# Kernel optimization log

Measured on AMD Instinct MI355X. Metric: run time of the kernel, lower is better.

Reference implementation:

```python
import jax, jax.numpy as jnp
import numpy as np

B, N_NODE, E_PER, C, HID, HEADS, IN, NL = 16, 1024, 8192, 16, 128, 4, 32, 2
N = B * N_NODE
NEG_SLOPE = 0.2


def setup_inputs() -> dict:
    key = jax.random.key(0)
    ks = jax.random.split(key, 16)
    obs = jax.random.normal(ks[0], (N, IN), jnp.float32)
    # per-graph random edges, guaranteed no self-loops (GATv2Conv re-adds them once)
    src_l = jax.random.randint(ks[1], (B, E_PER), 0, N_NODE)
    off = jax.random.randint(ks[2], (B, E_PER), 1, N_NODE)
    dst_l = (src_l + off) % N_NODE
    base = (jnp.arange(B) * N_NODE)[:, None]
    edge_index = jnp.stack([(src_l + base).reshape(-1), (dst_l + base).reshape(-1)]).astype(jnp.int32)

    def lin(k, fi, fo):
        return (jax.random.normal(k, (fi, fo), jnp.float32) / np.sqrt(fi)).astype(jnp.float32)

    def gat(k):
        sk = jax.random.split(k, 3)
        return {
            'Wl': (jax.random.normal(sk[0], (NL, HID, HEADS * HID), jnp.float32) / np.sqrt(HID)),
            'bl': jnp.zeros((NL, HEADS * HID), jnp.float32),
            'Wr': (jax.random.normal(sk[1], (NL, HID, HEADS * HID), jnp.float32) / np.sqrt(HID)),
            'br': jnp.zeros((NL, HEADS * HID), jnp.float32),
            'att': (jax.random.normal(sk[2], (NL, HEADS, HID), jnp.float32) / np.sqrt(HID)),
            'bias': jnp.zeros((NL, HID), jnp.float32),
            'g': jnp.ones((NL, HID), jnp.float32),
            'beta': jnp.zeros((NL, HID), jnp.float32),
        }

    inp = {'obs': obs, 'edge_index': edge_index, 'n_node': N_NODE,
           'emb_W': lin(ks[3], IN, HID), 'emb_b': jnp.zeros((HID,), jnp.float32),
           'pool_W': lin(ks[4], HID, C), 'pool_b': jnp.zeros((C,), jnp.float32),
           'mlp_W1': lin(ks[5], HID, 4 * HID), 'mlp_b1': jnp.zeros((4 * HID,), jnp.float32),
           'mlp_W2': lin(ks[6], 4 * HID, HID), 'mlp_b2': jnp.zeros((HID,), jnp.float32)}
    for nm, d in (('low', gat(ks[7])), ('high', gat(ks[8]))):
        for k2, v in d.items():
            inp[nm + '_' + k2] = v
    return inp


def _layer_norm(x, g, b):
    mu = x.mean(-1, keepdims=True)
    v = jnp.mean((x - mu) ** 2, -1, keepdims=True)
    return (x - mu) / jnp.sqrt(v + 1e-5) * g + b


def _gatv2(x, src, dst, Wl, bl, Wr, br, att, bias):
    # GATv2Conv: heads H, concat=False (mean over heads), eval mode (no dropout)
    n = x.shape[0]
    H, D = att.shape
    xl = (x @ Wl + bl).reshape(n, H, D)  # source transform (lin_l)
    xr = (x @ Wr + br).reshape(n, H, D)  # target transform (lin_r)
    e = jax.nn.leaky_relu(xl[src] + xr[dst], NEG_SLOPE)  # [E,H,D]
    logit = jnp.einsum('ehd,hd->eh', e, att)
    m = jax.ops.segment_max(logit, dst, num_segments=n)
    p = jnp.exp(logit - m[dst])
    z = jax.ops.segment_sum(p, dst, num_segments=n)
    alpha = p / z[dst]
    out = jax.ops.segment_sum(alpha[:, :, None] * xl[src], dst, num_segments=n)
    return out.mean(axis=1) + bias


def _gat_stack(h, src, dst, Wl, bl, Wr, br, att, bias, g, beta):
    h_res = h
    nl = Wl.shape[0]
    for j in range(nl):
        h_in = h
        h = _gatv2(h, src, dst, Wl[j], bl[j], Wr[j], br[j], att[j], bias[j])
        h = _layer_norm(h, g[j], beta[j])
        if j != nl - 1:
            h = jax.nn.silu(h)
        h = h + h_in  # use_res=True
    return h + h_res


def _forward(obs, edge_index, n_node, emb_W, emb_b, pool_W, pool_b, mlp_W1, mlp_b1, mlp_W2, mlp_b2,
             low_Wl, low_bl, low_Wr, low_br, low_att, low_bias, low_g, low_beta,
             high_Wl, high_bl, high_Wr, high_br, high_att, high_bias, high_g, high_beta):
    n = obs.shape[0]
    h = obs @ emb_W + emb_b
    hh = h
    # low-level edges + self-loops (GATv2Conv add_self_loops; input has none)
    loops = jnp.arange(n, dtype=edge_index.dtype)
    src = jnp.concatenate([edge_index[0], loops])
    dst = jnp.concatenate([edge_index[1], loops])
    h = _gat_stack(h, src, dst, low_Wl, low_bl, low_Wr, low_br, low_att, low_bias, low_g, low_beta)
    # soft pooling
    pooling = jax.nn.softmax(h @ pool_W + pool_b, axis=-1)  # dim=1 == last dim on 2D
    b = n // n_node
    c = pooling.shape[-1]
    s = pooling.reshape(b, n_node, c)
    count = jnp.maximum(s.sum(axis=1), 1e-5)  # sT @ ones, clamp_min(1e-5)
    Hf = jnp.einsum('bnc,bnd->bcd', s, h.reshape(b, n_node, -1)) / count[:, :, None]
    Hf = Hf.reshape(b * c, -1)
    # high-level: fully connected per-graph cluster edges (self-loops already present once)
    hr = jnp.repeat(jnp.arange(c, dtype=jnp.int32), c)
    hc = jnp.tile(jnp.arange(c, dtype=jnp.int32), c)
    offb = (jnp.arange(b, dtype=jnp.int32) * c)[:, None]
    hsrc = (hr[None, :] + offb).reshape(-1)
    hdst = (hc[None, :] + offb).reshape(-1)
    Hf = _gat_stack(Hf, hsrc, hdst, high_Wl, high_bl, high_Wr, high_br, high_att, high_bias, high_g, high_beta)
    # unpool + residual MLP (BaseMLP flat=True: hidden=4*HID, Tanh, residual)
    l_H = jnp.einsum('bnc,bcd->bnd', s, Hf.reshape(b, c, -1)).reshape(n, -1)
    x = l_H + hh
    return jnp.tanh(x @ mlp_W1 + mlp_b1) @ mlp_W2 + mlp_b2 + x


def reference(obs, edge_index, n_node, emb_W, emb_b, pool_W, pool_b, mlp_W1, mlp_b1, mlp_W2, mlp_b2,
              low_Wl, low_bl, low_Wr, low_br, low_att, low_bias, low_g, low_beta,
              high_Wl, high_bl, high_Wr, high_br, high_att, high_bias, high_g, high_beta):
    return _forward(obs, edge_index, n_node, emb_W, emb_b, pool_W, pool_b, mlp_W1, mlp_b1, mlp_W2, mlp_b2,
                    low_Wl, low_bl, low_Wr, low_br, low_att, low_bias, low_g, low_beta,
                    high_Wl, high_bl, high_Wr, high_br, high_att, high_bias, high_g, high_beta)
```

## Files before the change

kernel.cpp:

```cpp
#include <hip/hip_runtime.h>
#include <math.h>

#define NTOT  16384
#define NNODE 1024

typedef unsigned short u16;
typedef unsigned short u16x8 __attribute__((ext_vector_type(8)));
typedef short s16x8 __attribute__((ext_vector_type(8)));
typedef float f32x4 __attribute__((ext_vector_type(4)));

static __device__ __forceinline__ float b2f(u16 u) {
  return __uint_as_float(((unsigned)u) << 16);
}
static __device__ __forceinline__ u16 f2b(float f) {
  unsigned x = __float_as_uint(f);
  return (u16)((x + 0x7FFFu + ((x >> 16) & 1u)) >> 16);
}

__global__ __launch_bounds__(64) void emb_k(const float* __restrict__ obs,
    const float* __restrict__ W, const float* __restrict__ b,
    float* __restrict__ h, float* __restrict__ hh, u16* __restrict__ h_bf)
{
  int n = blockIdx.x, l = threadIdx.x;
  __shared__ float ob[32];
  if (l < 32) ob[l] = obs[n * 32 + l];
  __syncthreads();
  float a0 = b[l], a1 = b[64 + l];
  #pragma unroll
  for (int k = 0; k < 32; ++k) {
    float o = ob[k];
    a0 = fmaf(o, W[k * 128 + l], a0);
    a1 = fmaf(o, W[k * 128 + 64 + l], a1);
  }
  size_t base = (size_t)n * 128;
  h[base + l] = a0;  h[base + 64 + l] = a1;
  hh[base + l] = a0; hh[base + 64 + l] = a1;
  h_bf[base + l] = f2b(a0); h_bf[base + 64 + l] = f2b(a1);
}

__global__ void hist_k(const int* __restrict__ ei, int E0, int* __restrict__ deg)
{
  int i = blockIdx.x * blockDim.x + threadIdx.x;
  int ET = E0 + NTOT;
  if (i < ET) {
    int d = (i < E0) ? ei[E0 + i] : (i - E0);
    atomicAdd(&deg[d], 1);
  }
}

__global__ __launch_bounds__(256) void scan_k(const int* __restrict__ deg,
    int* __restrict__ off, int* __restrict__ cursor)
{
  __shared__ int part[256];
  int t = threadIdx.x;
  int base = t * 64;
  int sum = 0;
  for (int i = 0; i < 64; ++i) sum += deg[base + i];
  part[t] = sum;
  __syncthreads();
  if (t == 0) {
    int run = 0;
    for (int i = 0; i < 256; ++i) { int v = part[i]; part[i] = run; run += v; }
  }
  __syncthreads();
  int run = part[t];
  for (int i = 0; i < 64; ++i) {
    off[base + i] = run; cursor[base + i] = run;
    run += deg[base + i];
  }
  if (t == 255) off[NTOT] = run;
}

__global__ void scat_k(const int* __restrict__ ei, int E0,
    int* __restrict__ cursor, int* __restrict__ csr_src)
{
  int i = blockIdx.x * blockDim.x + threadIdx.x;
  int ET = E0 + NTOT;
  if (i < ET) {
    int s, d;
    if (i < E0) { s = ei[i]; d = ei[E0 + i]; } else { s = d = i - E0; }
    int pos = atomicAdd(&cursor[d], 1);
    csr_src[pos] = s;
  }
}

__global__ void hi_k(int* __restrict__ hi_off, int* __restrict__ hi_src)
{
  int t = threadIdx.x;
  hi_off[t] = t * 16;
  if (t == 0) hi_off[256] = 4096;
  for (int i = t; i < 4096; i += 256) {
    int u = i >> 4;
    hi_src[i] = (u & ~15) + (i & 15);
  }
}

__global__ void wq_k(const float* __restrict__ W, u16* __restrict__ out,
                     int K, int N, int total)
{
  int idx = blockIdx.x * 256 + threadIdx.x;
  if (idx >= total) return;
  int kn = K * N;
  int m = idx / kn, r = idx - m * kn;
  int n = r / K, k = r - n * K;
  out[idx] = f2b(W[(size_t)m * kn + (size_t)k * N + n]);
}

__global__ void wq2_k(const float* __restrict__ Wl, const float* __restrict__ Wr,
                      u16* __restrict__ out, int total)
{
  int idx = blockIdx.x * 256 + threadIdx.x;
  if (idx >= total) return;
  int m = idx >> 17;
  int r = idx & 131071;
  int n = r >> 7, k = r & 127;
  const float* W = (n < 512) ? Wl : Wr;
  out[idx] = f2b(W[(size_t)m * 65536 + (size_t)k * 512 + (n & 511)]);
}

__global__ __launch_bounds__(256) void gemm_bf16(
    const u16* __restrict__ A, const u16* __restrict__ Bt,
    const float* __restrict__ bias0, const float* __restrict__ bias1,
    float* __restrict__ Cf, u16* __restrict__ Cb0, u16* __restrict__ Cb1,
    const float* __restrict__ res,
    int M, int K, int N, int Nsplit, int act)
{
  __shared__ u16 Al[128][128];
  __shared__ u16 Bl[128][128];
  const int tid = threadIdx.x;
  const int bm = blockIdx.x * 128, bn = blockIdx.y * 128;
  const int w = tid >> 6, l = tid & 63;
  const int fr = l & 15;
  const int kg = l >> 4;
  const int sr = tid >> 1;
  const int sh = (tid & 1) << 3;

  f32x4 acc[2][8];
  #pragma unroll
  for (int a = 0; a < 2; ++a)
    #pragma unroll
    for (int b = 0; b < 8; ++b)
      acc[a][b] = (f32x4){0.f, 0.f, 0.f, 0.f};

  for (int k0 = 0; k0 < K; k0 += 128) {
    __syncthreads();
    const u16* As = A + (size_t)(bm + sr) * K + k0 + (sh << 3);
    const u16* Bs = Bt + (size_t)(bn + sr) * K + k0 + (sh << 3);
    #pragma unroll
    for (int i = 0; i < 8; ++i) {
      int gs = (sh + i) ^ (sr & 7);
      *(uint4*)&Al[sr][gs << 3] = *(const uint4*)(As + (i << 3));
    }
    #pragma unroll
    for (int i = 0; i < 8; ++i) {
      int gs = (sh + i) ^ (sr & 7);
      *(uint4*)&Bl[sr][gs << 3] = *(const uint4*)(Bs + (i << 3));
    }
    __syncthreads();
    #pragma unroll
    for (int ks = 0; ks < 4; ++ks) {
      const int g = (ks << 2) + kg;
      const int ar0 = w * 32 + fr, ar1 = ar0 + 16;
      s16x8 a0 = *(const s16x8*)&Al[ar0][(g ^ (ar0 & 7)) << 3];
      s16x8 a1 = *(const s16x8*)&Al[ar1][(g ^ (ar1 & 7)) << 3];
      #pragma unroll
      for (int nr = 0; nr < 8; ++nr) {
        const int br = nr * 16 + fr;
        s16x8 bb = *(const s16x8*)&Bl[br][(g ^ (br & 7)) << 3];
        acc[0][nr] = __builtin_amdgcn_mfma_f32_16x16x32_bf16(a0, bb, acc[0][nr], 0, 0, 0);
        acc[1][nr] = __builtin_amdgcn_mfma_f32_16x16x32_bf16(a1, bb, acc[1][nr], 0, 0, 0);
      }
    }
  }

  #pragma unroll
  for (int mr = 0; mr < 2; ++mr) {
    const int row0 = bm + w * 32 + mr * 16 + (kg << 2);
    #pragma unroll
    for (int nr = 0; nr < 8; ++nr) {
      const int col = bn + nr * 16 + fr;
      const int half = (col >= Nsplit);
      const int c2 = half ? col - Nsplit : col;
      const int str = half ? (N - Nsplit) : Nsplit;
      const float bb = half ? bias1[c2] : bias0[c2];
      u16* cb = half ? Cb1 : Cb0;
      #pragma unroll
      for (int j = 0; j < 4; ++j) {
        float v = acc[mr][nr][j] + bb;
        if (act) v = tanhf(v);
        size_t o = (size_t)(row0 + j) * str + c2;
        if (res) v += res[o];
        if (Cf) Cf[o] = v;
        if (cb) cb[o] = f2b(v);
      }
    }
  }
}

static __device__ __forceinline__ void edge_step(
    u16x8 vv, bool valid, const float* xrr, const float* attr,
    float& m, float& z, float* acc)
{
  float xv[8];
  #pragma unroll
  for (int i = 0; i < 8; ++i) xv[i] = b2f(vv[i]);
  float part = 0.f;
  #pragma unroll
  for (int i = 0; i < 8; ++i) {
    float v = xv[i] + xrr[i];
    part = fmaf(fmaxf(v, 0.2f * v), attr[i], part);
  }
  part += __shfl_xor(part, 1); part += __shfl_xor(part, 2);
  part += __shfl_xor(part, 4); part += __shfl_xor(part, 8);
  if (!valid) part = -1e30f;
  float mn = fmaxf(m, part);
  float sc = __expf(m - mn);
  float p  = __expf(part - mn);
  z = z * sc + p;
  #pragma unroll
  for (int i = 0; i < 8; ++i) acc[i] = fmaf(acc[i], sc, p * xv[i]);
  m = mn;
}

__global__ __launch_bounds__(64) void gat_agg2(
    const u16* __restrict__ xl, const u16* __restrict__ xr,
    const int* __restrict__ off, const int* __restrict__ srcs,
    const float* __restrict__ att, const float* __restrict__ bias,
    const float* __restrict__ g, const float* __restrict__ beta,
    float* __restrict__ h, u16* __restrict__ h_bf,
    const float* __restrict__ res2, int do_silu, int swz)
{
  int b = blockIdx.x, l = threadIdx.x;
  int dst0;
  if (swz) {
    int xcd = b & 7, i = b >> 3;
    dst0 = (((xcd << 1) + (i >> 9)) << 10) | ((i & 511) << 1);
  } else dst0 = b << 1;
  const int dst1 = dst0 + 1;

  float attr[8];
  {
    const float4 a0 = *(const float4*)(att + l * 8);
    const float4 a1 = *(const float4*)(att + l * 8 + 4);
    attr[0] = a0.x; attr[1] = a0.y; attr[2] = a0.z; attr[3] = a0.w;
    attr[4] = a1.x; attr[5] = a1.y; attr[6] = a1.z; attr[7] = a1.w;
  }
  float xrr0[8], xrr1[8];
  {
    u16x8 v0 = *(const u16x8*)(xr + (size_t)dst0 * 512 + l * 8);
    u16x8 v1 = *(const u16x8*)(xr + (size_t)dst1 * 512 + l * 8);
    #pragma unroll
    for (int i = 0; i < 8; ++i) { xrr0[i] = b2f(v0[i]); xrr1[i] = b2f(v1[i]); }
  }
  const int s0 = off[dst0], n0 = off[dst0 + 1] - s0;
  const int s1 = off[dst1], n1 = off[dst1 + 1] - s1;
  const int nmax = n0 > n1 ? n0 : n1;

  int ni0 = (n0 > 1) ? srcs[s0 + 1] : 0;
  int ni1 = (n1 > 1) ? srcs[s1 + 1] : 0;
  u16x8 v0 = *(const u16x8*)(xl + (size_t)srcs[s0] * 512 + l * 8);
  u16x8 v1 = *(const u16x8*)(xl + (size_t)srcs[s1] * 512 + l * 8);

  float m0 = -1e30f, z0 = 0.f, acc0[8] = {};
  float m1 = -1e30f, z1 = 0.f, acc1[8] = {};

  for (int e = 0; e < nmax; ++e) {
    u16x8 c0 = v0, c1 = v1;
    if (e + 1 < nmax) {
      v0 = *(const u16x8*)(xl + (size_t)ni0 * 512 + l * 8);
      v1 = *(const u16x8*)(xl + (size_t)ni1 * 512 + l * 8);
      if (e + 2 < n0) ni0 = srcs[s0 + e + 2];
      if (e + 2 < n1) ni1 = srcs[s1 + e + 2];
    }
    edge_step(c0, e < n0, xrr0, attr, m0, z0, acc0);
    edge_step(c1, e < n1, xrr1, attr, m1, z1, acc1);
  }

  const int d0 = (l & 15) * 8;
  float o0[8], o1[8];
  const float inv0 = 0.25f / z0, inv1 = 0.25f / z1;
  #pragma unroll
  for (int i = 0; i < 8; ++i) {
    float v = acc0[i] * inv0;
    v += __shfl_xor(v, 16); v += __shfl_xor(v, 32);
    o0[i] = v + bias[d0 + i];
    float w2 = acc1[i] * inv1;
    w2 += __shfl_xor(w2, 16); w2 += __shfl_xor(w2, 32);
    o1[i] = w2 + bias[d0 + i];
  }
  float sa = 0.f, sb = 0.f;
  #pragma unroll
  for (int i = 0; i < 8; ++i) { sa += o0[i]; sb += o1[i]; }
  sa += __shfl_xor(sa, 1); sa += __shfl_xor(sa, 2);
  sa += __shfl_xor(sa, 4); sa += __shfl_xor(sa, 8);
  sb += __shfl_xor(sb, 1); sb += __shfl_xor(sb, 2);
  sb += __shfl_xor(sb, 4); sb += __shfl_xor(sb, 8);
  const float mu0 = sa * (1.f / 128.f), mu1 = sb * (1.f / 128.f);
  float va = 0.f, vb = 0.f;
  #pragma unroll
  for (int i = 0; i < 8; ++i) {
    float d = o0[i] - mu0; va += d * d;
    float e = o1[i] - mu1; vb += e * e;
  }
  va += __shfl_xor(va, 1); va += __shfl_xor(va, 2);
  va += __shfl_xor(va, 4); va += __shfl_xor(va, 8);
  vb += __shfl_xor(vb, 1); vb += __shfl_xor(vb, 2);
  vb += __shfl_xor(vb, 4); vb += __shfl_xor(vb, 8);
  const float rstd0 = rsqrtf(va * (1.f / 128.f) + 1e-5f);
  const float rstd1 = rsqrtf(vb * (1.f / 128.f) + 1e-5f);

  const float* oo = (l < 16) ? o0 : o1;
  const float mu = (l < 16) ? mu0 : mu1;
  const float rstd = (l < 16) ? rstd0 : rstd1;
  const int dd = (l < 16) ? dst0 : dst1;
  if (l < 32) {
    size_t base = (size_t)dd * 128 + d0;
    float4 r0 = *(const float4*)(h + base);
    float4 r1 = *(const float4*)(h + base + 4);
    float rr[8] = {r0.x, r0.y, r0.z, r0.w, r1.x, r1.y, r1.z, r1.w};
    if (res2) {
      float4 q0 = *(const float4*)(res2 + base);
      float4 q1 = *(const float4*)(res2 + base + 4);
      rr[0] += q0.x; rr[1] += q0.y; rr[2] += q0.z; rr[3] += q0.w;
      rr[4] += q1.x; rr[5] += q1.y; rr[6] += q1.z; rr[7] += q1.w;
    }
    float out[8];
    u16x8 hb;
    #pragma unroll
    for (int i = 0; i < 8; ++i) {
      float y = (oo[i] - mu) * rstd * g[d0 + i] + beta[d0 + i];
      if (do_silu) y = y / (1.f + __expf(-y));
      out[i] = y + rr[i];
      hb[i] = f2b(out[i]);
    }
    *(float4*)(h + base) = make_float4(out[0], out[1], out[2], out[3]);
    *(float4*)(h + base + 4) = make_float4(out[4], out[5], out[6], out[7]);
    *(u16x8*)(h_bf + base) = hb;
  }
}

__global__ __launch_bounds__(256) void pool_k(const float* __restrict__ h,
    const float* __restrict__ W, const float* __restrict__ b, float* __restrict__ s)
{
  __shared__ float hs[16 * 130];
  __shared__ float Ws[128 * 16];
  int t = threadIdx.x;
  int n0 = blockIdx.x * 16;
  #pragma unroll
  for (int i = 0; i < 8; ++i) {
    int idx = t + 256 * i;
    hs[(idx >> 7) * 130 + (idx & 127)] = h[(size_t)n0 * 128 + idx];
    Ws[idx] = W[idx];
  }
  __syncthreads();
  int nl = t >> 4, c = t & 15;
  float acc = b[c];
  for (int k = 0; k < 128; ++k) acc = fmaf(hs[nl * 130 + k], Ws[k * 16 + c], acc);
  float mx = acc;
  mx = fmaxf(mx, __shfl_xor(mx, 1)); mx = fmaxf(mx, __shfl_xor(mx, 2));
  mx = fmaxf(mx, __shfl_xor(mx, 4)); mx = fmaxf(mx, __shfl_xor(mx, 8));
  float p = __expf(acc - mx), sum = p;
  sum += __shfl_xor(sum, 1); sum += __shfl_xor(sum, 2);
  sum += __shfl_xor(sum, 4); sum += __shfl_xor(sum, 8);
  s[(size_t)(n0 + nl) * 16 + c] = p / sum;
}

#define HF_CHUNK 32
#define HF_NCH   32
__global__ __launch_bounds__(256) void hfp_k(const float* __restrict__ s,
    const float* __restrict__ h, float* __restrict__ part, float* __restrict__ cpart)
{
  __shared__ float ss[HF_CHUNK][16];
  __shared__ float hs[HF_CHUNK][128];
  int b = blockIdx.x >> 5, chunk = blockIdx.x & 31;
  int n0 = b * NNODE + chunk * HF_CHUNK;
  int t = threadIdx.x;
  if (t < 128) {
    float4 v = *(const float4*)(s + (size_t)(n0 + (t >> 2)) * 16 + (t & 3) * 4);
    *(float4*)&ss[t >> 2][(t & 3) * 4] = v;
  }
  #pragma unroll
  for (int i = 0; i < 4; ++i) {
    int idx = t + 256 * i;
    int row = idx >> 5, c4 = (idx & 31) * 4;
    *(float4*)&hs[row][c4] = *(const float4*)(h + (size_t)(n0 + row) * 128 + c4);
  }
  __syncthreads();
  int d = t & 127, cg = (t >> 7) * 8;
  float acc[8] = {};
  for (int n = 0; n < HF_CHUNK; ++n) {
    float hv = hs[n][d];
    #pragma unroll
    for (int i = 0; i < 8; ++i) acc[i] = fmaf(ss[n][cg + i], hv, acc[i]);
  }
  float* po = part + (size_t)chunk * 32768 + (size_t)(b * 16 + cg) * 128 + d;
  #pragma unroll
  for (int i = 0; i < 8; ++i) po[i * 128] = acc[i];
  if (t < 16) {
    float c = 0.f;
    #pragma unroll
    for (int n = 0; n < HF_CHUNK; ++n) c += ss[n][t];
    cpart[chunk * 256 + b * 16 + t] = c;
  }
}

__global__ __launch_bounds__(256) void hfr_k(const float* __restrict__ part,
    const float* __restrict__ cpart, float* __restrict__ Hf,
    float* __restrict__ HfRes, u16* __restrict__ Hf_bf)
{
  int o = blockIdx.x * 256 + threadIdx.x;
  int bc = o >> 7;
  float a = 0.f, cnt = 0.f;
  #pragma unroll 8
  for (int ch = 0; ch < HF_NCH; ++ch) {
    a += part[(size_t)ch * 32768 + o];
    cnt += cpart[ch * 256 + bc];
  }
  float v = a / fmaxf(cnt, 1e-5f);
  Hf[o] = v; HfRes[o] = v; Hf_bf[o] = f2b(v);
}

__global__ __launch_bounds__(64) void unpool_k(const float* __restrict__ s,
    const float* __restrict__ Hf, const float* __restrict__ hh,
    float* __restrict__ x, u16* __restrict__ x_bf)
{
  int n = blockIdx.x, l = threadIdx.x;
  int b = n >> 10;
  float a0 = 0.f, a1 = 0.f;
  #pragma unroll
  for (int c = 0; c < 16; ++c) {
    float sv = s[(size_t)n * 16 + c];
    const float* hp = Hf + (size_t)((b << 4) + c) * 128;
    a0 = fmaf(sv, hp[l], a0);
    a1 = fmaf(sv, hp[64 + l], a1);
  }
  size_t base = (size_t)n * 128;
  float v0 = a0 + hh[base + l], v1 = a1 + hh[base + 64 + l];
  x[base + l] = v0; x[base + 64 + l] = v1;
  x_bf[base + l] = f2b(v0); x_bf[base + 64 + l] = f2b(v1);
}

extern "C" void kernel_launch(void* const* d_in, const int* in_sizes, int n_in,
                              void* d_out, int out_size, void* d_ws, size_t ws_size,
                              hipStream_t stream) {
  (void)n_in; (void)out_size; (void)ws_size;
  const float* obs    = (const float*)d_in[0];
  const int*   ei     = (const int*)d_in[1];
  const float* emb_W  = (const float*)d_in[3];
  const float* emb_b  = (const float*)d_in[4];
  const float* pool_W = (const float*)d_in[5];
  const float* pool_b = (const float*)d_in[6];
  const float* mlp_W1 = (const float*)d_in[7];
  const float* mlp_b1 = (const float*)d_in[8];
  const float* mlp_W2 = (const float*)d_in[9];
  const float* mlp_b2 = (const float*)d_in[10];
  const float* lWl = (const float*)d_in[11]; const float* lbl = (const float*)d_in[12];
  const float* lWr = (const float*)d_in[13]; const float* lbr = (const float*)d_in[14];
  const float* latt = (const float*)d_in[15]; const float* lbias = (const float*)d_in[16];
  const float* lg = (const float*)d_in[17]; const float* lbeta = (const float*)d_in[18];
  const float* hWl = (const float*)d_in[19]; const float* hbl = (const float*)d_in[20];
  const float* hWr = (const float*)d_in[21]; const float* hbr = (const float*)d_in[22];
  const float* hatt = (const float*)d_in[23]; const float* hbias = (const float*)d_in[24];
  const float* hg = (const float*)d_in[25]; const float* hbeta = (const float*)d_in[26];

  const int E0 = in_sizes[1] / 2;
  const int ET = E0 + NTOT;

  char* p = (char*)d_ws;
  auto alloc = [&](size_t bytes) -> void* {
    void* q = (void*)p;
    p += (bytes + 255) & ~(size_t)255;
    return q;
  };
  float* h      = (float*)alloc((size_t)NTOT * 128 * 4);
  float* hh     = (float*)alloc((size_t)NTOT * 128 * 4);
  u16*   h_bf   = (u16*)alloc((size_t)NTOT * 128 * 2);
  u16*   xl_bf  = (u16*)alloc((size_t)NTOT * 512 * 2);
  u16*   xr_bf  = (u16*)alloc((size_t)NTOT * 512 * 2);
  u16*   x_bf   = (u16*)alloc((size_t)NTOT * 128 * 2);
  float* s      = (float*)alloc((size_t)NTOT * 16 * 4);
  float* Hf     = (float*)alloc(256 * 128 * 4);
  float* HfRes  = (float*)alloc(256 * 128 * 4);
  u16*   Hf_bf  = (u16*)alloc(256 * 128 * 2);
  u16*   hxl    = (u16*)alloc(256 * 512 * 2);
  u16*   hxr    = (u16*)alloc(256 * 512 * 2);
  float* hfPart = (float*)alloc((size_t)HF_NCH * 32768 * 4);
  float* hfCnt  = (float*)alloc((size_t)HF_NCH * 256 * 4);
  u16*   lWT    = (u16*)alloc(2 * 1024 * 128 * 2);
  u16*   hWT    = (u16*)alloc(2 * 1024 * 128 * 2);
  u16*   W1T    = (u16*)alloc(512 * 128 * 2);
  u16*   W2T    = (u16*)alloc(128 * 512 * 2);
  int* deg      = (int*)alloc((size_t)NTOT * 4);
  int* off      = (int*)alloc((size_t)(NTOT + 1) * 4);
  int* cursor   = (int*)alloc((size_t)NTOT * 4);
  int* csr      = (int*)alloc((size_t)ET * 4);
  int* hi_off   = (int*)alloc(257 * 4);
  int* hi_src   = (int*)alloc(4096 * 4);
  u16* t_bf     = xl_bf;

  wq2_k<<<(2 * 131072 + 255) / 256, 256, 0, stream>>>(lWl, lWr, lWT, 2 * 131072);
  wq2_k<<<(2 * 131072 + 255) / 256, 256, 0, stream>>>(hWl, hWr, hWT, 2 * 131072);
  wq_k<<<(65536 + 255) / 256, 256, 0, stream>>>(mlp_W1, W1T, 128, 512, 65536);
  wq_k<<<(65536 + 255) / 256, 256, 0, stream>>>(mlp_W2, W2T, 512, 128, 65536);

  hipMemsetAsync(deg, 0, (size_t)NTOT * 4, stream);
  emb_k<<<NTOT, 64, 0, stream>>>(obs, emb_W, emb_b, h, hh, h_bf);
  hist_k<<<(ET + 255) / 256, 256, 0, stream>>>(ei, E0, deg);
  scan_k<<<1, 256, 0, stream>>>(deg, off, cursor);
  scat_k<<<(ET + 255) / 256, 256, 0, stream>>>(ei, E0, cursor, csr);
  hi_k<<<1, 256, 0, stream>>>(hi_off, hi_src);

  for (int j = 0; j < 2; ++j) {
    gemm_bf16<<<dim3(NTOT / 128, 8), 256, 0, stream>>>(h_bf, lWT + j * 131072,
        lbl + j * 512, lbr + j * 512, nullptr, xl_bf, xr_bf, nullptr,
        NTOT, 128, 1024, 512, 0);
    gat_agg2<<<NTOT / 2, 64, 0, stream>>>(xl_bf, xr_bf, off, csr, latt + j * 512,
        lbias + j * 128, lg + j * 128, lbeta + j * 128, h, h_bf,
        j == 1 ? hh : nullptr, j == 0 ? 1 : 0, 1);
  }

  pool_k<<<NTOT / 16, 256, 0, stream>>>(h, pool_W, pool_b, s);
  hfp_k<<<16 * HF_NCH, 256, 0, stream>>>(s, h, hfPart, hfCnt);
  hfr_k<<<128, 256, 0, stream>>>(hfPart, hfCnt, Hf, HfRes, Hf_bf);

  for (int j = 0; j < 2; ++j) {
    gemm_bf16<<<dim3(2, 8), 256, 0, stream>>>(Hf_bf, hWT + j * 131072,
        hbl + j * 512, hbr + j * 512, nullptr, hxl, hxr, nullptr,
        256, 128, 1024, 512, 0);
    gat_agg2<<<128, 64, 0, stream>>>(hxl, hxr, hi_off, hi_src, hatt + j * 512,
        hbias + j * 128, hg + j * 128, hbeta + j * 128, Hf, Hf_bf,
        j == 1 ? HfRes : nullptr, j == 0 ? 1 : 0, 0);
  }

  float* x = (float*)d_out;
  unpool_k<<<NTOT, 64, 0, stream>>>(s, Hf, hh, x, x_bf);
  gemm_bf16<<<dim3(NTOT / 128, 4), 256, 0, stream>>>(x_bf, W1T, mlp_b1, nullptr,
      nullptr, t_bf, nullptr, nullptr, NTOT, 128, 512, 512, 1);
  gemm_bf16<<<dim3(NTOT / 128, 1), 256, 0, stream>>>(t_bf, W2T, mlp_b2, nullptr,
      x, nullptr, nullptr, x, NTOT, 512, 128, 128, 0);
}
```

Before: 398.6 us.

## Batch GAT aggregation, use global_load_lds in GEMMs, fuse pool and weight prep

Several independent changes land together. The GEMM tile loads now use global_load_lds, which writes straight into LDS instead of going through registers. A 64-row GEMM variant is added for the small high-level GEMMs and for the second MLP GEMM. The low-level GAT aggregation now handles 4 destination nodes per wave instead of 2, and the high-level GAT uses a dedicated fully connected 16-node kernel in place of the CSR tables. The softmax pool is fused into the Hf partial-sum kernel, the four weight-conversion kernels become one launch, and the scan uses wave shuffles. These changes cut launch count and register traffic, at the cost of more registers per thread and more divergence from uneven node degrees within each 4-node batch.

After: 404.7 us. About the same (+1.5%).

```diff
diff --git a/kernel.cpp b/kernel.cpp
--- a/kernel.cpp
+++ b/kernel.cpp
@@ -15,6 +15,12 @@
 static __device__ __forceinline__ u16 f2b(float f) {
   unsigned x = __float_as_uint(f);
   return (u16)((x + 0x7FFFu + ((x >> 16) & 1u)) >> 16);
+}
+
+typedef __attribute__((address_space(1))) const void gvoid;
+typedef __attribute__((address_space(3))) void lvoid;
+static __device__ __forceinline__ void gload16(const void* g, void* lds) {
+  __builtin_amdgcn_global_load_lds((gvoid*)g, (lvoid*)lds, 16, 0, 0);
 }
 
 __global__ __launch_bounds__(64) void emb_k(const float* __restrict__ obs,
@@ -51,19 +57,22 @@
 __global__ __launch_bounds__(256) void scan_k(const int* __restrict__ deg,
     int* __restrict__ off, int* __restrict__ cursor)
 {
-  __shared__ int part[256];
-  int t = threadIdx.x;
+  int t = threadIdx.x, lane = t & 63, wid = t >> 6;
   int base = t * 64;
   int sum = 0;
   for (int i = 0; i < 64; ++i) sum += deg[base + i];
-  part[t] = sum;
+  int inc = sum;
+  #pragma unroll
+  for (int d = 1; d < 64; d <<= 1) {
+    int u = __shfl_up(inc, d);
+    if (lane >= d) inc += u;
+  }
+  __shared__ int wt[4];
+  if (lane == 63) wt[wid] = inc;
   __syncthreads();
-  if (t == 0) {
-    int run = 0;
-    for (int i = 0; i < 256; ++i) { int v = part[i]; part[i] = run; run += v; }
-  }
-  __syncthreads();
-  int run = part[t];
+  int woff = 0;
+  for (int i = 0; i < wid; ++i) woff += wt[i];
+  int run = woff + inc - sum;
   for (int i = 0; i < 64; ++i) {
     off[base + i] = run; cursor[base + i] = run;
     run += deg[base + i];
@@ -84,38 +93,32 @@
   }
 }
 
-__global__ void hi_k(int* __restrict__ hi_off, int* __restrict__ hi_src)
-{
-  int t = threadIdx.x;
-  hi_off[t] = t * 16;
-  if (t == 0) hi_off[256] = 4096;
-  for (int i = t; i < 4096; i += 256) {
-    int u = i >> 4;
-    hi_src[i] = (u & ~15) + (i & 15);
-  }
-}
-
-__global__ void wq_k(const float* __restrict__ W, u16* __restrict__ out,
-                     int K, int N, int total)
+__global__ void wqall_k(const float* __restrict__ lWl, const float* __restrict__ lWr,
+                        const float* __restrict__ hWl, const float* __restrict__ hWr,
+                        const float* __restrict__ W1, const float* __restrict__ W2,
+                        u16* __restrict__ out)
 {
   int idx = blockIdx.x * 256 + threadIdx.x;
-  if (idx >= total) return;
-  int kn = K * N;
-  int m = idx / kn, r = idx - m * kn;
-  int n = r / K, k = r - n * K;
-  out[idx] = f2b(W[(size_t)m * kn + (size_t)k * N + n]);
-}
-
-__global__ void wq2_k(const float* __restrict__ Wl, const float* __restrict__ Wr,
-                      u16* __restrict__ out, int total)
-{
-  int idx = blockIdx.x * 256 + threadIdx.x;
-  if (idx >= total) return;
-  int m = idx >> 17;
-  int r = idx & 131071;
-  int n = r >> 7, k = r & 127;
-  const float* W = (n < 512) ? Wl : Wr;
-  out[idx] = f2b(W[(size_t)m * 65536 + (size_t)k * 512 + (n & 511)]);
+  if (idx >= 655360) return;
+  float v;
+  if (idx < 524288) {
+    const float* Wl = idx < 262144 ? lWl : hWl;
+    const float* Wr = idx < 262144 ? lWr : hWr;
+    int r2 = idx & 262143;
+    int m = r2 >> 17, r = r2 & 131071;
+    int n = r >> 7, k = r & 127;
+    const float* W = (n < 512) ? Wl : Wr;
+    v = W[(size_t)m * 65536 + (size_t)k * 512 + (n & 511)];
+  } else if (idx < 589824) {
+    int i = idx - 524288;
+    int n = i >> 7, k = i & 127;
+    v = W1[k * 512 + n];
+  } else {
+    int i = idx - 589824;
+    int n = i >> 9, k = i & 511;
+    v = W2[k * 128 + n];
+  }
+  out[idx] = f2b(v);
 }
 
 __global__ __launch_bounds__(256) void gemm_bf16(
@@ -132,8 +135,7 @@
   const int w = tid >> 6, l = tid & 63;
   const int fr = l & 15;
   const int kg = l >> 4;
-  const int sr = tid >> 1;
-  const int sh = (tid & 1) << 3;
+  const int lrow = l >> 4, gsl = l & 15;
 
   f32x4 acc[2][8];
   #pragma unroll
@@ -144,17 +146,17 @@
 
   for (int k0 = 0; k0 < K; k0 += 128) {
     __syncthreads();
-    const u16* As = A + (size_t)(bm + sr) * K + k0 + (sh << 3);
-    const u16* Bs = Bt + (size_t)(bn + sr) * K + k0 + (sh << 3);
-    #pragma unroll
-    for (int i = 0; i < 8; ++i) {
-      int gs = (sh + i) ^ (sr & 7);
-      *(uint4*)&Al[sr][gs << 3] = *(const uint4*)(As + (i << 3));
-    }
-    #pragma unroll
-    for (int i = 0; i < 8; ++i) {
-      int gs = (sh + i) ^ (sr & 7);
-      *(uint4*)&Bl[sr][gs << 3] = *(const uint4*)(Bs + (i << 3));
+    #pragma unroll
+    for (int j = 0; j < 8; ++j) {
+      int row = w * 32 + j * 4 + lrow;
+      int gsrc = gsl ^ (row & 7);
+      gload16(A + (size_t)(bm + row) * K + k0 + gsrc * 8, &Al[w * 32 + j * 4][0]);
+    }
+    #pragma unroll
+    for (int j = 0; j < 8; ++j) {
+      int row = w * 32 + j * 4 + lrow;
+      int gsrc = gsl ^ (row & 7);
+      gload16(Bt + (size_t)(bn + row) * K + k0 + gsrc * 8, &Bl[w * 32 + j * 4][0]);
     }
     __syncthreads();
     #pragma unroll
@@ -197,17 +199,85 @@
   }
 }
 
-static __device__ __forceinline__ void edge_step(
-    u16x8 vv, bool valid, const float* xrr, const float* attr,
+__global__ __launch_bounds__(256) void gemm64_bf16(
+    const u16* __restrict__ A, const u16* __restrict__ Bt,
+    const float* __restrict__ bias0, const float* __restrict__ bias1,
+    float* __restrict__ Cf, u16* __restrict__ Cb0, u16* __restrict__ Cb1,
+    const float* __restrict__ res,
+    int M, int K, int N, int Nsplit, int act)
+{
+  __shared__ u16 Al[64][128];
+  __shared__ u16 Bl[128][128];
+  const int tid = threadIdx.x;
+  const int bm = blockIdx.x * 64, bn = blockIdx.y * 128;
+  const int w = tid >> 6, l = tid & 63;
+  const int fr = l & 15;
+  const int kg = l >> 4;
+  const int lrow = l >> 4, gsl = l & 15;
+
+  f32x4 acc[8];
+  #pragma unroll
+  for (int b = 0; b < 8; ++b) acc[b] = (f32x4){0.f, 0.f, 0.f, 0.f};
+
+  for (int k0 = 0; k0 < K; k0 += 128) {
+    __syncthreads();
+    #pragma unroll
+    for (int j = 0; j < 4; ++j) {
+      int row = w * 16 + j * 4 + lrow;
+      int gsrc = gsl ^ (row & 7);
+      gload16(A + (size_t)(bm + row) * K + k0 + gsrc * 8, &Al[w * 16 + j * 4][0]);
+    }
+    #pragma unroll
+    for (int j = 0; j < 8; ++j) {
+      int row = w * 32 + j * 4 + lrow;
+      int gsrc = gsl ^ (row & 7);
+      gload16(Bt + (size_t)(bn + row) * K + k0 + gsrc * 8, &Bl[w * 32 + j * 4][0]);
+    }
+    __syncthreads();
+    #pragma unroll
+    for (int ks = 0; ks < 4; ++ks) {
+      const int g = (ks << 2) + kg;
+      const int ar0 = w * 16 + fr;
+      s16x8 a0 = *(const s16x8*)&Al[ar0][(g ^ (ar0 & 7)) << 3];
+      #pragma unroll
+      for (int nr = 0; nr < 8; ++nr) {
+        const int br = nr * 16 + fr;
+        s16x8 bb = *(const s16x8*)&Bl[br][(g ^ (br & 7)) << 3];
+        acc[nr] = __builtin_amdgcn_mfma_f32_16x16x32_bf16(a0, bb, acc[nr], 0, 0, 0);
+      }
+    }
+  }
+
+  const int row0 = bm + w * 16 + (kg << 2);
+  #pragma unroll
+  for (int nr = 0; nr < 8; ++nr) {
+    const int col = bn + nr * 16 + fr;
+    const int half = (col >= Nsplit);
+    const int c2 = half ? col - Nsplit : col;
+    const int str = half ? (N - Nsplit) : Nsplit;
+    const float bb = half ? bias1[c2] : bias0[c2];
+    u16* cb = half ? Cb1 : Cb0;
+    #pragma unroll
+    for (int j = 0; j < 4; ++j) {
+      float v = acc[nr][j] + bb;
+      if (act) v = tanhf(v);
+      size_t o = (size_t)(row0 + j) * str + c2;
+      if (res) v += res[o];
+      if (Cf) Cf[o] = v;
+      if (cb) cb[o] = f2b(v);
+    }
+  }
+}
+
+static __device__ __forceinline__ void estep(
+    u16x8 vv, bool valid, u16x8 xrb, const float* attr,
     float& m, float& z, float* acc)
 {
-  float xv[8];
-  #pragma unroll
-  for (int i = 0; i < 8; ++i) xv[i] = b2f(vv[i]);
-  float part = 0.f;
+  float xv[8], part = 0.f;
   #pragma unroll
   for (int i = 0; i < 8; ++i) {
-    float v = xv[i] + xrr[i];
+    xv[i] = b2f(vv[i]);
+    float v = xv[i] + b2f(xrb[i]);
     part = fmaf(fmaxf(v, 0.2f * v), attr[i], part);
   }
   part += __shfl_xor(part, 1); part += __shfl_xor(part, 2);
@@ -222,7 +292,7 @@
   m = mn;
 }
 
-__global__ __launch_bounds__(64) void gat_agg2(
+__global__ __launch_bounds__(64, 4) void gat_agg4(
     const u16* __restrict__ xl, const u16* __restrict__ xr,
     const int* __restrict__ off, const int* __restrict__ srcs,
     const float* __restrict__ att, const float* __restrict__ bias,
@@ -234,9 +304,8 @@
   int dst0;
   if (swz) {
     int xcd = b & 7, i = b >> 3;
-    dst0 = (((xcd << 1) + (i >> 9)) << 10) | ((i & 511) << 1);
-  } else dst0 = b << 1;
-  const int dst1 = dst0 + 1;
+    dst0 = (((xcd << 1) + (i >> 8)) << 10) | ((i & 255) << 2);
+  } else dst0 = b << 2;
 
   float attr[8];
   {
@@ -245,148 +314,235 @@
     attr[0] = a0.x; attr[1] = a0.y; attr[2] = a0.z; attr[3] = a0.w;
     attr[4] = a1.x; attr[5] = a1.y; attr[6] = a1.z; attr[7] = a1.w;
   }
-  float xrr0[8], xrr1[8];
+  u16x8 xrb[4];
+  #pragma unroll
+  for (int q = 0; q < 4; ++q)
+    xrb[q] = *(const u16x8*)(xr + (size_t)(dst0 + q) * 512 + l * 8);
+
+  int sE[4], nE[4];
+  #pragma unroll
+  for (int q = 0; q < 4; ++q) { sE[q] = off[dst0 + q]; nE[q] = off[dst0 + q + 1] - sE[q]; }
+  int nmax = nE[0] > nE[1] ? nE[0] : nE[1];
+  nmax = nmax > nE[2] ? nmax : nE[2];
+  nmax = nmax > nE[3] ? nmax : nE[3];
+
+  u16x8 v[4]; int ni[4];
+  #pragma unroll
+  for (int q = 0; q < 4; ++q) {
+    v[q] = *(const u16x8*)(xl + (size_t)srcs[sE[q]] * 512 + l * 8);
+    ni[q] = (nE[q] > 1) ? srcs[sE[q] + 1] : 0;
+  }
+  float m[4] = {-1e30f, -1e30f, -1e30f, -1e30f};
+  float z[4] = {0.f, 0.f, 0.f, 0.f};
+  float acc[4][8] = {};
+
+  for (int e = 0; e < nmax; ++e) {
+    u16x8 c0 = v[0], c1 = v[1], c2 = v[2], c3 = v[3];
+    if (e + 1 < nmax) {
+      #pragma unroll
+      for (int q = 0; q < 4; ++q)
+        v[q] = *(const u16x8*)(xl + (size_t)ni[q] * 512 + l * 8);
+      #pragma unroll
+      for (int q = 0; q < 4; ++q)
+        if (e + 2 < nE[q]) ni[q] = srcs[sE[q] + e + 2];
+    }
+    estep(c0, e < nE[0], xrb[0], attr, m[0], z[0], acc[0]);
+    estep(c1, e < nE[1], xrb[1], attr, m[1], z[1], acc[1]);
+    estep(c2, e < nE[2], xrb[2], attr, m[2], z[2], acc[2]);
+    estep(c3, e < nE[3], xrb[3], attr, m[3], z[3], acc[3]);
+  }
+
+  const int d0 = (l & 15) * 8;
+  float mu[4], rs[4];
+  #pragma unroll
+  for (int q = 0; q < 4; ++q) {
+    const float inv = 0.25f / z[q];
+    #pragma unroll
+    for (int i = 0; i < 8; ++i) {
+      float x = acc[q][i] * inv;
+      x += __shfl_xor(x, 16); x += __shfl_xor(x, 32);
+      acc[q][i] = x + bias[d0 + i];
+    }
+    float sa = 0.f;
+    #pragma unroll
+    for (int i = 0; i < 8; ++i) sa += acc[q][i];
+    sa += __shfl_xor(sa, 1); sa += __shfl_xor(sa, 2);
+    sa += __shfl_xor(sa, 4); sa += __shfl_xor(sa, 8);
+    mu[q] = sa * (1.f / 128.f);
+    float va = 0.f;
+    #pragma unroll
+    for (int i = 0; i < 8; ++i) { float d = acc[q][i] - mu[q]; va += d * d; }
+    va += __shfl_xor(va, 1); va += __shfl_xor(va, 2);
+    va += __shfl_xor(va, 4); va += __shfl_xor(va, 8);
+    rs[q] = rsqrtf(va * (1.f / 128.f) + 1e-5f);
+  }
+  float oo[8];
+  #pragma unroll
+  for (int i = 0; i < 8; ++i)
+    oo[i] = (l < 32) ? (l < 16 ? acc[0][i] : acc[1][i])
+                     : (l < 48 ? acc[2][i] : acc[3][i]);
+  const float mmu = (l < 32) ? (l < 16 ? mu[0] : mu[1]) : (l < 48 ? mu[2] : mu[3]);
+  const float mrs = (l < 32) ? (l < 16 ? rs[0] : rs[1]) : (l < 48 ? rs[2] : rs[3]);
+  const int dd = dst0 + (l >> 4);
+  size_t base = (size_t)dd * 128 + d0;
+  float4 r0 = *(const float4*)(h + base);
+  float4 r1 = *(const float4*)(h + base + 4);
+  float rr[8] = {r0.x, r0.y, r0.z, r0.w, r1.x, r1.y, r1.z, r1.w};
+  if (res2) {
+    float4 q0 = *(const float4*)(res2 + base);
+    float4 q1 = *(const float4*)(res2 + base + 4);
+    rr[0] += q0.x; rr[1] += q0.y; rr[2] += q0.z; rr[3] += q0.w;
+    rr[4] += q1.x; rr[5] += q1.y; rr[6] += q1.z; rr[7] += q1.w;
+  }
+  float out[8];
+  u16x8 hb;
+  #pragma unroll
+  for (int i = 0; i < 8; ++i) {
+    float y = (oo[i] - mmu) * mrs * g[d0 + i] + beta[d0 + i];
+    if (do_silu) y = y / (1.f + __expf(-y));
+    out[i] = y + rr[i];
+    hb[i] = f2b(out[i]);
+  }
+  *(float4*)(h + base) = make_float4(out[0], out[1], out[2], out[3]);
+  *(float4*)(h + base + 4) = make_float4(out[4], out[5], out[6], out[7]);
+  *(u16x8*)(h_bf + base) = hb;
+}
+
+__global__ __launch_bounds__(64) void gat_fc16(
+    const u16* __restrict__ xl, const u16* __restrict__ xr,
+    const float* __restrict__ att, const float* __restrict__ bias,
+    const float* __restrict__ g, const float* __restrict__ beta,
+    float* __restrict__ h, u16* __restrict__ h_bf,
+    const float* __restrict__ res2, int do_silu)
+{
+  int b = blockIdx.x, l = threadIdx.x;
+  const int dst0 = b << 2;
+  const int gbase = dst0 & ~15;
+
+  float attr[8];
   {
-    u16x8 v0 = *(const u16x8*)(xr + (size_t)dst0 * 512 + l * 8);
-    u16x8 v1 = *(const u16x8*)(xr + (size_t)dst1 * 512 + l * 8);
-    #pragma unroll
-    for (int i = 0; i < 8; ++i) { xrr0[i] = b2f(v0[i]); xrr1[i] = b2f(v1[i]); }
-  }
-  const int s0 = off[dst0], n0 = off[dst0 + 1] - s0;
-  const int s1 = off[dst1], n1 = off[dst1 + 1] - s1;
-  const int nmax = n0 > n1 ? n0 : n1;
-
-  int ni0 = (n0 > 1) ? srcs[s0 + 1] : 0;
-  int ni1 = (n1 > 1) ? srcs[s1 + 1] : 0;
-  u16x8 v0 = *(const u16x8*)(xl + (size_t)srcs[s0] * 512 + l * 8);
-  u16x8 v1 = *(const u16x8*)(xl + (size_t)srcs[s1] * 512 + l * 8);
-
-  float m0 = -1e30f, z0 = 0.f, acc0[8] = {};
-  float m1 = -1e30f, z1 = 0.f, acc1[8] = {};
-
-  for (int e = 0; e < nmax; ++e) {
-    u16x8 c0 = v0, c1 = v1;
-    if (e + 1 < nmax) {
-      v0 = *(const u16x8*)(xl + (size_t)ni0 * 512 + l * 8);
-      v1 = *(const u16x8*)(xl + (size_t)ni1 * 512 + l * 8);
-      if (e + 2 < n0) ni0 = srcs[s0 + e + 2];
-      if (e + 2 < n1) ni1 = srcs[s1 + e + 2];
-    }
-    edge_step(c0, e < n0, xrr0, attr, m0, z0, acc0);
-    edge_step(c1, e < n1, xrr1, attr, m1, z1, acc1);
+    const float4 a0 = *(const float4*)(att + l * 8);
+    const float4 a1 = *(const float4*)(att + l * 8 + 4);
+    attr[0] = a0.x; attr[1] = a0.y; attr[2] = a0.z; attr[3] = a0.w;
+    attr[4] = a1.x; attr[5] = a1.y; attr[6] = a1.z; attr[7] = a1.w;
+  }
+  u16x8 xrb[4];
+  #pragma unroll
+  for (int q = 0; q < 4; ++q)
+    xrb[q] = *(const u16x8*)(xr + (size_t)(dst0 + q) * 512 + l * 8);
+
+  float m[4] = {-1e30f, -1e30f, -1e30f, -1e30f};
+  float z[4] = {0.f, 0.f, 0.f, 0.f};
+  float acc[4][8] = {};
+  u16x8 vcur = *(const u16x8*)(xl + (size_t)gbase * 512 + l * 8);
+  for (int e = 0; e < 16; ++e) {
+    u16x8 c = vcur;
+    if (e < 15) vcur = *(const u16x8*)(xl + (size_t)(gbase + e + 1) * 512 + l * 8);
+    estep(c, true, xrb[0], attr, m[0], z[0], acc[0]);
+    estep(c, true, xrb[1], attr, m[1], z[1], acc[1]);
+    estep(c, true, xrb[2], attr, m[2], z[2], acc[2]);
+    estep(c, true, xrb[3], attr, m[3], z[3], acc[3]);
   }
 
   const int d0 = (l & 15) * 8;
-  float o0[8], o1[8];
-  const float inv0 = 0.25f / z0, inv1 = 0.25f / z1;
+  float mu[4], rs[4];
+  #pragma unroll
+  for (int q = 0; q < 4; ++q) {
+    const float inv = 0.25f / z[q];
+    #pragma unroll
+    for (int i = 0; i < 8; ++i) {
+      float x = acc[q][i] * inv;
+      x += __shfl_xor(x, 16); x += __shfl_xor(x, 32);
+      acc[q][i] = x + bias[d0 + i];
+    }
+    float sa = 0.f;
+    #pragma unroll
+    for (int i = 0; i < 8; ++i) sa += acc[q][i];
+    sa += __shfl_xor(sa, 1); sa += __shfl_xor(sa, 2);
+    sa += __shfl_xor(sa, 4); sa += __shfl_xor(sa, 8);
+    mu[q] = sa * (1.f / 128.f);
+    float va = 0.f;
+    #pragma unroll
+    for (int i = 0; i < 8; ++i) { float d = acc[q][i] - mu[q]; va += d * d; }
+    va += __shfl_xor(va, 1); va += __shfl_xor(va, 2);
+    va += __shfl_xor(va, 4); va += __shfl_xor(va, 8);
+    rs[q] = rsqrtf(va * (1.f / 128.f) + 1e-5f);
+  }
+  float oo[8];
+  #pragma unroll
+  for (int i = 0; i < 8; ++i)
+    oo[i] = (l < 32) ? (l < 16 ? acc[0][i] : acc[1][i])
+                     : (l < 48 ? acc[2][i] : acc[3][i]);
+  const float mmu = (l < 32) ? (l < 16 ? mu[0] : mu[1]) : (l < 48 ? mu[2] : mu[3]);
+  const float mrs = (l < 32) ? (l < 16 ? rs[0] : rs[1]) : (l < 48 ? rs[2] : rs[3]);
+  const int dd = dst0 + (l >> 4);
+  size_t base = (size_t)dd * 128 + d0;
+  float4 r0 = *(const float4*)(h + base);
+  float4 r1 = *(const float4*)(h + base + 4);
+  float rr[8] = {r0.x, r0.y, r0.z, r0.w, r1.x, r1.y, r1.z, r1.w};
+  if (res2) {
+    float4 q0 = *(const float4*)(res2 + base);
+    float4 q1 = *(const float4*)(res2 + base + 4);
+    rr[0] += q0.x; rr[1] += q0.y; rr[2] += q0.z; rr[3] += q0.w;
+    rr[4] += q1.x; rr[5] += q1.y; rr[6] += q1.z; rr[7] += q1.w;
+  }
+  float out[8];
+  u16x8 hb;
   #pragma unroll
   for (int i = 0; i < 8; ++i) {
-    float v = acc0[i] * inv0;
-    v += __shfl_xor(v, 16); v += __shfl_xor(v, 32);
-    o0[i] = v + bias[d0 + i];
-    float w2 = acc1[i] * inv1;
-    w2 += __shfl_xor(w2, 16); w2 += __shfl_xor(w2, 32);
-    o1[i] = w2 + bias[d0 + i];
-  }
-  float sa = 0.f, sb = 0.f;
-  #pragma unroll
-  for (int i = 0; i < 8; ++i) { sa += o0[i]; sb += o1[i]; }
-  sa += __shfl_xor(sa, 1); sa += __shfl_xor(sa, 2);
-  sa += __shfl_xor(sa, 4); sa += __shfl_xor(sa, 8);
-  sb += __shfl_xor(sb, 1); sb += __shfl_xor(sb, 2);
-  sb += __shfl_xor(sb, 4); sb += __shfl_xor(sb, 8);
-  const float mu0 = sa * (1.f / 128.f), mu1 = sb * (1.f / 128.f);
-  float va = 0.f, vb = 0.f;
-  #pragma unroll
-  for (int i = 0; i < 8; ++i) {
-    float d = o0[i] - mu0; va += d * d;
-    float e = o1[i] - mu1; vb += e * e;
-  }
-  va += __shfl_xor(va, 1); va += __shfl_xor(va, 2);
-  va += __shfl_xor(va, 4); va += __shfl_xor(va, 8);
-  vb += __shfl_xor(vb, 1); vb += __shfl_xor(vb, 2);
-  vb += __shfl_xor(vb, 4); vb += __shfl_xor(vb, 8);
-  const float rstd0 = rsqrtf(va * (1.f / 128.f) + 1e-5f);
-  const float rstd1 = rsqrtf(vb * (1.f / 128.f) + 1e-5f);
-
-  const float* oo = (l < 16) ? o0 : o1;
-  const float mu = (l < 16) ? mu0 : mu1;
-  const float rstd = (l < 16) ? rstd0 : rstd1;
-  const int dd = (l < 16) ? dst0 : dst1;
-  if (l < 32) {
-    size_t base = (size_t)dd * 128 + d0;
-    float4 r0 = *(const float4*)(h + base);
-    float4 r1 = *(const float4*)(h + base + 4);
-    float rr[8] = {r0.x, r0.y, r0.z, r0.w, r1.x, r1.y, r1.z, r1.w};
-    if (res2) {
-      float4 q0 = *(const float4*)(res2 + base);
-      float4 q1 = *(const float4*)(res2 + base + 4);
-      rr[0] += q0.x; rr[1] += q0.y; rr[2] += q0.z; rr[3] += q0.w;
-      rr[4] += q1.x; rr[5] += q1.y; rr[6] += q1.z; rr[7] += q1.w;
-    }
-    float out[8];
-    u16x8 hb;
-    #pragma unroll
-    for (int i = 0; i < 8; ++i) {
-      float y = (oo[i] - mu) * rstd * g[d0 + i] + beta[d0 + i];
-      if (do_silu) y = y / (1.f + __expf(-y));
-      out[i] = y + rr[i];
-      hb[i] = f2b(out[i]);
-    }
-    *(float4*)(h + base) = make_float4(out[0], out[1], out[2], out[3]);
-    *(float4*)(h + base + 4) = make_float4(out[4], out[5], out[6], out[7]);
-    *(u16x8*)(h_bf + base) = hb;
-  }
-}
-
-__global__ __launch_bounds__(256) void pool_k(const float* __restrict__ h,
-    const float* __restrict__ W, const float* __restrict__ b, float* __restrict__ s)
-{
-  __shared__ float hs[16 * 130];
-  __shared__ float Ws[128 * 16];
-  int t = threadIdx.x;
-  int n0 = blockIdx.x * 16;
-  #pragma unroll
-  for (int i = 0; i < 8; ++i) {
-    int idx = t + 256 * i;
-    hs[(idx >> 7) * 130 + (idx & 127)] = h[(size_t)n0 * 128 + idx];
-    Ws[idx] = W[idx];
-  }
-  __syncthreads();
-  int nl = t >> 4, c = t & 15;
-  float acc = b[c];
-  for (int k = 0; k < 128; ++k) acc = fmaf(hs[nl * 130 + k], Ws[k * 16 + c], acc);
-  float mx = acc;
-  mx = fmaxf(mx, __shfl_xor(mx, 1)); mx = fmaxf(mx, __shfl_xor(mx, 2));
-  mx = fmaxf(mx, __shfl_xor(mx, 4)); mx = fmaxf(mx, __shfl_xor(mx, 8));
-  float p = __expf(acc - mx), sum = p;
-  sum += __shfl_xor(sum, 1); sum += __shfl_xor(sum, 2);
-  sum += __shfl_xor(sum, 4); sum += __shfl_xor(sum, 8);
-  s[(size_t)(n0 + nl) * 16 + c] = p / sum;
+    float y = (oo[i] - mmu) * mrs * g[d0 + i] + beta[d0 + i];
+    if (do_silu) y = y / (1.f + __expf(-y));
+    out[i] = y + rr[i];
+    hb[i] = f2b(out[i]);
+  }
+  *(float4*)(h + base) = make_float4(out[0], out[1], out[2], out[3]);
+  *(float4*)(h + base + 4) = make_float4(out[4], out[5], out[6], out[7]);
+  *(u16x8*)(h_bf + base) = hb;
 }
 
 #define HF_CHUNK 32
 #define HF_NCH   32
-__global__ __launch_bounds__(256) void hfp_k(const float* __restrict__ s,
-    const float* __restrict__ h, float* __restrict__ part, float* __restrict__ cpart)
-{
+__global__ __launch_bounds__(256) void poolhf_k(const float* __restrict__ h,
+    const float* __restrict__ pW, const float* __restrict__ pb,
+    float* __restrict__ s, float* __restrict__ part, float* __restrict__ cpart)
+{
+  __shared__ float hs[HF_CHUNK][128];
+  __shared__ float Ws[128][16];
   __shared__ float ss[HF_CHUNK][16];
-  __shared__ float hs[HF_CHUNK][128];
   int b = blockIdx.x >> 5, chunk = blockIdx.x & 31;
   int n0 = b * NNODE + chunk * HF_CHUNK;
   int t = threadIdx.x;
-  if (t < 128) {
-    float4 v = *(const float4*)(s + (size_t)(n0 + (t >> 2)) * 16 + (t & 3) * 4);
-    *(float4*)&ss[t >> 2][(t & 3) * 4] = v;
-  }
   #pragma unroll
   for (int i = 0; i < 4; ++i) {
     int idx = t + 256 * i;
     int row = idx >> 5, c4 = (idx & 31) * 4;
     *(float4*)&hs[row][c4] = *(const float4*)(h + (size_t)(n0 + row) * 128 + c4);
   }
+  #pragma unroll
+  for (int i = 0; i < 2; ++i) {
+    int idx = t + 256 * i;
+    *(float4*)&Ws[idx >> 2][(idx & 3) * 4] = *(const float4*)(pW + idx * 4);
+  }
   __syncthreads();
-  int d = t & 127, cg = (t >> 7) * 8;
+  const int c = t & 15, nA = t >> 4;
+  const float bb = pb[c];
+  #pragma unroll
+  for (int half = 0; half < 2; ++half) {
+    const int nn = nA + half * 16;
+    float a = bb;
+    for (int k = 0; k < 128; ++k) a = fmaf(hs[nn][k], Ws[k][c], a);
+    float mx = a;
+    mx = fmaxf(mx, __shfl_xor(mx, 1)); mx = fmaxf(mx, __shfl_xor(mx, 2));
+    mx = fmaxf(mx, __shfl_xor(mx, 4)); mx = fmaxf(mx, __shfl_xor(mx, 8));
+    float p = __expf(a - mx), sum = p;
+    sum += __shfl_xor(sum, 1); sum += __shfl_xor(sum, 2);
+    sum += __shfl_xor(sum, 4); sum += __shfl_xor(sum, 8);
+    float sv = p / sum;
+    ss[nn][c] = sv;
+    s[(size_t)(n0 + nn) * 16 + c] = sv;
+  }
+  __syncthreads();
+  const int d = t & 127, cg = (t >> 7) * 8;
   float acc[8] = {};
   for (int n = 0; n < HF_CHUNK; ++n) {
     float hv = hs[n][d];
@@ -397,10 +553,10 @@
   #pragma unroll
   for (int i = 0; i < 8; ++i) po[i * 128] = acc[i];
   if (t < 16) {
-    float c = 0.f;
-    #pragma unroll
-    for (int n = 0; n < HF_CHUNK; ++n) c += ss[n][t];
-    cpart[chunk * 256 + b * 16 + t] = c;
+    float cs = 0.f;
+    #pragma unroll
+    for (int n = 0; n < HF_CHUNK; ++n) cs += ss[n][t];
+    cpart[chunk * 256 + b * 16 + t] = cs;
   }
 }
 
@@ -486,56 +642,50 @@
   u16*   hxr    = (u16*)alloc(256 * 512 * 2);
   float* hfPart = (float*)alloc((size_t)HF_NCH * 32768 * 4);
   float* hfCnt  = (float*)alloc((size_t)HF_NCH * 256 * 4);
-  u16*   lWT    = (u16*)alloc(2 * 1024 * 128 * 2);
-  u16*   hWT    = (u16*)alloc(2 * 1024 * 128 * 2);
-  u16*   W1T    = (u16*)alloc(512 * 128 * 2);
-  u16*   W2T    = (u16*)alloc(128 * 512 * 2);
+  u16*   WT     = (u16*)alloc((size_t)655360 * 2);
   int* deg      = (int*)alloc((size_t)NTOT * 4);
   int* off      = (int*)alloc((size_t)(NTOT + 1) * 4);
   int* cursor   = (int*)alloc((size_t)NTOT * 4);
   int* csr      = (int*)alloc((size_t)ET * 4);
-  int* hi_off   = (int*)alloc(257 * 4);
-  int* hi_src   = (int*)alloc(4096 * 4);
-  u16* t_bf     = xl_bf;
-
-  wq2_k<<<(2 * 131072 + 255) / 256, 256, 0, stream>>>(lWl, lWr, lWT, 2 * 131072);
-  wq2_k<<<(2 * 131072 + 255) / 256, 256, 0, stream>>>(hWl, hWr, hWT, 2 * 131072);
-  wq_k<<<(65536 + 255) / 256, 256, 0, stream>>>(mlp_W1, W1T, 128, 512, 65536);
-  wq_k<<<(65536 + 255) / 256, 256, 0, stream>>>(mlp_W2, W2T, 512, 128, 65536);
+  u16* lWT = WT;
+  u16* hWT = WT + 262144;
+  u16* W1T = WT + 524288;
+  u16* W2T = WT + 589824;
+  u16* t_bf = xl_bf;
+
+  wqall_k<<<2560, 256, 0, stream>>>(lWl, lWr, hWl, hWr, mlp_W1, mlp_W2, WT);
 
   hipMemsetAsync(deg, 0, (size_t)NTOT * 4, stream);
   emb_k<<<NTOT, 64, 0, stream>>>(obs, emb_W, emb_b, h, hh, h_bf);
   hist_k<<<(ET + 255) / 256, 256, 0, stream>>>(ei, E0, deg);
   scan_k<<<1, 256, 0, stream>>>(deg, off, cursor);
   scat_k<<<(ET + 255) / 256, 256, 0, stream>>>(ei, E0, cursor, csr);
-  hi_k<<<1, 256, 0, stream>>>(hi_off, hi_src);
 
   for (int j = 0; j < 2; ++j) {
     gemm_bf16<<<dim3(NTOT / 128, 8), 256, 0, stream>>>(h_bf, lWT + j * 131072,
         lbl + j * 512, lbr + j * 512, nullptr, xl_bf, xr_bf, nullptr,
         NTOT, 128, 1024, 512, 0);
-    gat_agg2<<<NTOT / 2, 64, 0, stream>>>(xl_bf, xr_bf, off, csr, latt + j * 512,
+    gat_agg4<<<NTOT / 4, 64, 0, stream>>>(xl_bf, xr_bf, off, csr, latt + j * 512,
         lbias + j * 128, lg + j * 128, lbeta + j * 128, h, h_bf,
         j == 1 ? hh : nullptr, j == 0 ? 1 : 0, 1);
   }
 
-  pool_k<<<NTOT / 16, 256, 0, stream>>>(h, pool_W, pool_b, s);
-  hfp_k<<<16 * HF_NCH, 256, 0, stream>>>(s, h, hfPart, hfCnt);
+  poolhf_k<<<16 * HF_NCH, 256, 0, stream>>>(h, pool_W, pool_b, s, hfPart, hfCnt);
   hfr_k<<<128, 256, 0, stream>>>(hfPart, hfCnt, Hf, HfRes, Hf_bf);
 
   for (int j = 0; j < 2; ++j) {
-    gemm_bf16<<<dim3(2, 8), 256, 0, stream>>>(Hf_bf, hWT + j * 131072,
+    gemm64_bf16<<<dim3(4, 8), 256, 0, stream>>>(Hf_bf, hWT + j * 131072,
         hbl + j * 512, hbr + j * 512, nullptr, hxl, hxr, nullptr,
         256, 128, 1024, 512, 0);
-    gat_agg2<<<128, 64, 0, stream>>>(hxl, hxr, hi_off, hi_src, hatt + j * 512,
-        hbias + j * 128, hg + j * 128, hbeta + j * 128, Hf, Hf_bf,
-        j == 1 ? HfRes : nullptr, j == 0 ? 1 : 0, 0);
+    gat_fc16<<<64, 64, 0, stream>>>(hxl, hxr, hatt + j * 512, hbias + j * 128,
+        hg + j * 128, hbeta + j * 128, Hf, Hf_bf,
+        j == 1 ? HfRes : nullptr, j == 0 ? 1 : 0);
   }
 
   float* x = (float*)d_out;
   unpool_k<<<NTOT, 64, 0, stream>>>(s, Hf, hh, x, x_bf);
-  gemm_bf16<<<dim3(NTOT / 128, 4), 256, 0, stream>>>(x_bf, W1T, mlp_b1, nullptr,
+  gemm_bf16<<<dim3(NTOT / 128, 4), 256, 0, stream>>>(x_bf, W1T, mlp_b1, mlp_b1,
       nullptr, t_bf, nullptr, nullptr, NTOT, 128, 512, 512, 1);
-  gemm_bf16<<<dim3(NTOT / 128, 1), 256, 0, stream>>>(t_bf, W2T, mlp_b2, nullptr,
+  gemm64_bf16<<<dim3(NTOT / 64, 1), 256, 0, stream>>>(t_bf, W2T, mlp_b2, mlp_b2,
       x, nullptr, nullptr, x, NTOT, 512, 128, 128, 0);
 }
```
